# Optimization experiments

Measured on AMD Instinct MI355X. Metric: run time of the kernel, lower is better.

Reference implementation:

```python
import jax, jax.numpy as jnp
import numpy as np

N, T, F, H, DEG = 1024, 32, 128, 4, 32
HID, OUT = 512, 64
NNZ = N * DEG
D = F // H


def setup_inputs() -> dict:
    key = jax.random.key(0)
    ks = jax.random.split(key, 40)
    p = lambda i, shape, s=0.05: (jax.random.normal(ks[i], shape, dtype=jnp.float32) * s)
    inp = {
        'A_rows': jnp.repeat(jnp.arange(N, dtype=jnp.int32), DEG),
        'A_cols': jax.random.randint(ks[0], (NNZ,), 0, N, dtype=jnp.int32),
        'A_vals': jax.random.uniform(ks[1], (NNZ,), dtype=jnp.float32) / DEG,
        'X': jax.random.normal(ks[2], (N, T, F), dtype=jnp.float32),
        'W_gcn': p(3, (F, F)),
        'W_ih': p(4, (3 * F, F)), 'W_hh': p(5, (3 * F, F)),
        'b_ih': p(6, (3 * F,)), 'b_hh': p(7, (3 * F,)),
        'in_proj_w': p(8, (3 * F, F)), 'in_proj_b': p(9, (3 * F,)),
        'out_proj_w': p(10, (F, F)), 'out_proj_b': p(11, (F,)),
        'ln1_g': jnp.ones((F,), jnp.float32), 'ln1_b': jnp.zeros((F,), jnp.float32),
        'ln2_g': jnp.ones((F,), jnp.float32), 'ln2_b': jnp.zeros((F,), jnp.float32),
        'lnf_g': jnp.ones((F,), jnp.float32), 'lnf_b': jnp.zeros((F,), jnp.float32),
        'ff1_w': p(12, (HID, F)), 'ff1_b': p(13, (HID,)),
        'ff2_w': p(14, (F, HID)), 'ff2_b': p(15, (F,)),
        'fc1_w': p(16, (HID, T * F)), 'fc1_b': p(17, (HID,)),
        'fc2_w': p(18, (HID, HID)), 'fc2_b': p(19, (HID,)),
        'fc3_w': p(20, (OUT, HID)), 'fc3_b': p(21, (OUT,)),
    }
    return inp


def _pos_encoding():
    # pe[i, t] = sin(t / 10000**(2i/F)) for even t, cos(...) for odd t; constant over feature dim.
    i = jnp.arange(N, dtype=jnp.float32)
    t = jnp.arange(T, dtype=jnp.float32)
    inv = jnp.exp(-(2.0 * i / F) * jnp.log(jnp.float32(10000.0)))  # [N]
    ang = t[None, :] * inv[:, None]                                # [N, T]
    even = (jnp.arange(T) % 2 == 0)[None, :]
    return jnp.where(even, jnp.sin(ang), jnp.cos(ang))             # [N, T]


def _layer_norm(x, g, b, eps=1e-5):
    mu = x.mean(-1, keepdims=True)
    var = ((x - mu) ** 2).mean(-1, keepdims=True)
    return (x - mu) * jax.lax.rsqrt(var + eps) * g + b


def _forward(A_rows, A_cols, A_vals, X, W_gcn, W_ih, W_hh, b_ih, b_hh,
             in_proj_w, in_proj_b, out_proj_w, out_proj_b,
             ln1_g, ln1_b, ln2_g, ln2_b, lnf_g, lnf_b,
             ff1_w, ff1_b, ff2_w, ff2_b,
             fc1_w, fc1_b, fc2_w, fc2_b, fc3_w, fc3_b):
    def spmm(x2d):  # A_hat @ x2d via COO gather + segment-sum
        return jax.ops.segment_sum(A_vals[:, None] * x2d[A_cols], A_rows, num_segments=N)

    def gru_cell(x, h):  # torch GRUCell, gate order [r; z; n]
        gi = x @ W_ih.T + b_ih
        gh = h @ W_hh.T + b_hh
        ir, iz, inn = jnp.split(gi, 3, axis=-1)
        hr, hz, hn = jnp.split(gh, 3, axis=-1)
        r = jax.nn.sigmoid(ir + hr)
        z = jax.nn.sigmoid(iz + hz)
        n = jnp.tanh(inn + r * hn)
        return (1.0 - z) * n + z * h

    # GCN on full [N, T, F] block
    X_tilde = jax.nn.relu(spmm(X.reshape(N, T * F)).reshape(N, T, F) @ W_gcn)

    # sequential GRU + per-step GCN over time
    def step(h, x_t):
        g = gru_cell(x_t, h)                       # [N, F]
        h_new = jax.nn.relu(spmm(g) @ W_gcn)
        return h_new, g

    h0 = jnp.zeros((N, F), X.dtype)
    _, Hs = jax.lax.scan(step, h0, jnp.transpose(X_tilde, (1, 0, 2)))  # [T, N, F]
    Hm = jnp.transpose(Hs, (1, 0, 2)) + _pos_encoding()[:, :, None]    # [N, T, F]

    # TransformerEncoderLayer (post-norm, relu, dropout=0); seq axis = nodes, batch axis = T
    qkv = Hm @ in_proj_w.T + in_proj_b                 # [N, T, 3F]
    q, k, v = jnp.split(qkv, 3, axis=-1)
    q = q.reshape(N, T, H, D) * (1.0 / jnp.sqrt(jnp.float32(D)))
    k = k.reshape(N, T, H, D)
    v = v.reshape(N, T, H, D)
    scores = jnp.einsum('nthd,mthd->thnm', q, k)       # [T, H, N, N]
    attn = jax.nn.softmax(scores, axis=-1)
    ctx = jnp.einsum('thnm,mthd->nthd', attn, v).reshape(N, T, F)
    attn_out = ctx @ out_proj_w.T + out_proj_b
    x1 = _layer_norm(Hm + attn_out, ln1_g, ln1_b)
    ff = jax.nn.relu(x1 @ ff1_w.T + ff1_b) @ ff2_w.T + ff2_b
    x2 = _layer_norm(x1 + ff, ln2_g, ln2_b)
    enc = _layer_norm(x2, lnf_g, lnf_b)                # final encoder norm

    # MLP head
    flat = enc.reshape(N, T * F)
    h1 = jax.nn.relu(flat @ fc1_w.T + fc1_b)
    h2 = jax.nn.relu(h1 @ fc2_w.T + fc2_b)
    return h2 @ fc3_w.T + fc3_b                        # [N, OUT]


def reference(A_rows, A_cols, A_vals, X, W_gcn, W_ih, W_hh, b_ih, b_hh,
              in_proj_w, in_proj_b, out_proj_w, out_proj_b,
              ln1_g, ln1_b, ln2_g, ln2_b, lnf_g, lnf_b,
              ff1_w, ff1_b, ff2_w, ff2_b,
              fc1_w, fc1_b, fc2_w, fc2_b, fc3_w, fc3_b):
    return _forward(A_rows, A_cols, A_vals, X, W_gcn, W_ih, W_hh, b_ih, b_hh,
                    in_proj_w, in_proj_b, out_proj_w, out_proj_b,
                    ln1_g, ln1_b, ln2_g, ln2_b, lnf_g, lnf_b,
                    ff1_w, ff1_b, ff2_w, ff2_b,
                    fc1_w, fc1_b, fc2_w, fc2_b, fc3_w, fc3_b)
```

## Files before the change

### kernel.cpp

```cpp
#include <hip/hip_runtime.h>
#include <hip/hip_bf16.h>
#include <math.h>

#define N_NODES 1024
#define T_STEPS 32
#define F_DIM   128
#define H_HEADS 4
#define D_HEAD  32
#define DEG     32
#define HID     512
#define OUT_DIM 64
#define TF      (T_STEPS * F_DIM)
#define NT      (N_NODES * T_STEPS)
#define F3      (3 * F_DIM)

typedef __attribute__((ext_vector_type(8))) __bf16 bf16x8;
typedef __attribute__((ext_vector_type(4))) float  f32x4;

__device__ __forceinline__ short f2bf(float x) {
    union { float f; unsigned u; } v; v.f = x;
    unsigned r = (v.u + 0x7FFFu + ((v.u >> 16) & 1u)) >> 16;
    return (short)r;
}

__global__ void zero_kernel(float* p, int n) {
    int i = blockIdx.x * 256 + threadIdx.x;
    if (i < n) p[i] = 0.f;
}

template <bool RELU>
__global__ void bias_act(float* __restrict__ C, const float* __restrict__ bias,
                         int P, int total) {
    int i = blockIdx.x * 256 + threadIdx.x;
    if (i < total) {
        float v = C[i] + bias[i & (P - 1)];
        if (RELU) v = fmaxf(v, 0.f);
        C[i] = v;
    }
}

__global__ void transpose_whh(const float* __restrict__ W, float* __restrict__ WT) {
    int idx = blockIdx.x * 256 + threadIdx.x;
    if (idx < F3 * F_DIM) {
        int j = idx / F_DIM;
        int k = idx % F_DIM;
        WT[k * F3 + j] = W[idx];
    }
}

__global__ void spmm_wide(const int* __restrict__ cols, const float* __restrict__ vals,
                          const float* __restrict__ X, float* __restrict__ Y) {
    int n = blockIdx.y;
    int c = blockIdx.x * 256 + threadIdx.x;
    const int*   ce = cols + n * DEG;
    const float* ve = vals + n * DEG;
    float acc = 0.f;
#pragma unroll
    for (int e = 0; e < DEG; ++e) acc += ve[e] * X[ce[e] * TF + c];
    Y[n * TF + c] = acc;
}

__global__ __launch_bounds__(256) void gates_kernel(
        const float* __restrict__ GI, const float* __restrict__ GH,
        const float* __restrict__ h, const float* __restrict__ b_hh,
        float* __restrict__ g_out, float* __restrict__ Hm, int t) {
    int idx = blockIdx.x * 256 + threadIdx.x;
    int n = idx >> 7, f = idx & 127;
    size_t gib = ((size_t)n * T_STEPS + t) * F3;
    size_t ghb = (size_t)n * F3;
    float ir  = GI[gib + f];
    float iz  = GI[gib + 128 + f];
    float inn = GI[gib + 256 + f];
    float hr  = GH[ghb + f]       + b_hh[f];
    float hz  = GH[ghb + 128 + f] + b_hh[128 + f];
    float hn  = GH[ghb + 256 + f] + b_hh[256 + f];
    float hv  = h[idx];
    float rr = 1.f / (1.f + expf(-(ir + hr)));
    float zz = 1.f / (1.f + expf(-(iz + hz)));
    float nn = tanhf(inn + rr * hn);
    float g  = (1.f - zz) * nn + zz * hv;
    g_out[idx] = g;
    float inv = __expf(-(float)n * (9.210340371976184f / 64.0f));
    float ang = (float)t * inv;
    float pe  = ((t & 1) == 0) ? sinf(ang) : cosf(ang);
    Hm[((size_t)n * T_STEPS + t) * F_DIM + f] = g + pe;
}

__global__ __launch_bounds__(256) void scan_step(
        const int* __restrict__ cols, const float* __restrict__ vals,
        const float* __restrict__ g_in, const float* __restrict__ Wg,
        const float* __restrict__ WhhT, const float* __restrict__ b_hh,
        const float* __restrict__ GI, float* __restrict__ g_out,
        float* __restrict__ Hm, int t_next) {
    __shared__ float sp[2][F_DIM];
    __shared__ float hsn[2][F_DIM];
    __shared__ float part[2][F_DIM][8];
    __shared__ float gpart[2][2][F_DIM];
    int tid = threadIdx.x;
    int n0 = blockIdx.x * 2;
    int f = tid & 127, half = tid >> 7;
    float b0 = 0.f, b1 = 0.f;
    int eb = half * 16;
#pragma unroll
    for (int e = 0; e < 16; ++e) {
        int i0 = n0 * DEG + eb + e;
        int i1 = (n0 + 1) * DEG + eb + e;
        b0 += vals[i0] * g_in[cols[i0] * F_DIM + f];
        b1 += vals[i1] * g_in[cols[i1] * F_DIM + f];
    }
    gpart[half][0][f] = b0; gpart[half][1][f] = b1;
    __syncthreads();
    sp[half][f] = gpart[0][half][f] + gpart[1][half][f];
    __syncthreads();
    float c0 = 0.f, c1 = 0.f;
    int kb = half * 64;
#pragma unroll 4
    for (int k = 0; k < 64; ++k) {
        int kk = kb + k;
        float w = Wg[kk * F_DIM + f];
        c0 += sp[0][kk] * w; c1 += sp[1][kk] * w;
    }
    gpart[half][0][f] = c0; gpart[half][1][f] = c1;
    __syncthreads();
    {
        float hv = fmaxf(gpart[0][half][f] + gpart[1][half][f], 0.f);
        hsn[half][f] = hv;
    }
    __syncthreads();
    float a[6] = {0.f, 0.f, 0.f, 0.f, 0.f, 0.f};
#pragma unroll 2
    for (int k = 0; k < 64; ++k) {
        int kk = kb + k;
        const float* w = WhhT + kk * F3;
        float wr = w[f], wz = w[128 + f], wn = w[256 + f];
        float h0 = hsn[0][kk], h1 = hsn[1][kk];
        a[0] += h0 * wr; a[1] += h0 * wz; a[2] += h0 * wn;
        a[3] += h1 * wr; a[4] += h1 * wz; a[5] += h1 * wn;
    }
#pragma unroll
    for (int i = 0; i < 6; ++i) part[half][f][i] = a[i];
    __syncthreads();
    {
        int node = n0 + half;
        float ghr = part[0][f][half * 3 + 0] + part[1][f][half * 3 + 0] + b_hh[f];
        float ghz = part[0][f][half * 3 + 1] + part[1][f][half * 3 + 1] + b_hh[128 + f];
        float ghn = part[0][f][half * 3 + 2] + part[1][f][half * 3 + 2] + b_hh[256 + f];
        size_t gib = ((size_t)node * T_STEPS + t_next) * F3;
        float hv = hsn[half][f];
        float rr = 1.f / (1.f + expf(-(GI[gib + f] + ghr)));
        float zz = 1.f / (1.f + expf(-(GI[gib + 128 + f] + ghz)));
        float nn = tanhf(GI[gib + 256 + f] + rr * ghn);
        float g  = (1.f - zz) * nn + zz * hv;
        g_out[node * F_DIM + f] = g;
        float inv = __expf(-(float)node * (9.210340371976184f / 64.0f));
        float ang = (float)t_next * inv;
        float pe  = ((t_next & 1) == 0) ? sinf(ang) : cosf(ang);
        Hm[((size_t)node * T_STEPS + t_next) * F_DIM + f] = g + pe;
    }
}

__global__ __launch_bounds__(256) void qkv_gemm(const float* __restrict__ A,
                                                const float* __restrict__ B,
                                                const float* __restrict__ bias,
                                                short* __restrict__ Qb,
                                                short* __restrict__ Kb,
                                                short* __restrict__ VTb) {
    __shared__ short As[64][40];
    __shared__ short Bs[64][40];
    int tid = threadIdx.x;
    int p0 = blockIdx.x * 64, row0 = blockIdx.y * 64;
    int lane = tid & 63, w = tid >> 6, col = lane & 15, quad = lane >> 4;
    f32x4 acc[4];
#pragma unroll
    for (int j = 0; j < 4; ++j) acc[j] = (f32x4){0.f, 0.f, 0.f, 0.f};
    for (int k0 = 0; k0 < F_DIM; k0 += 32) {
#pragma unroll
        for (int i = 0; i < 2; ++i) {
            int idx = tid * 2 + i;
            int r = idx >> 3, c4 = (idx & 7) << 2;
            const float4 f4 = *(const float4*)(A + (size_t)(row0 + r) * F_DIM + k0 + c4);
            union { __hip_bfloat162 h2[2]; short4 s4; } u;
            u.h2[0] = __float22bfloat162_rn(make_float2(f4.x, f4.y));
            u.h2[1] = __float22bfloat162_rn(make_float2(f4.z, f4.w));
            *(short4*)&As[r][c4] = u.s4;
        }
#pragma unroll
        for (int i = 0; i < 2; ++i) {
            int idx = tid * 2 + i;
            int r = idx >> 3, c4 = (idx & 7) << 2;
            const float4 f4 = *(const float4*)(B + (size_t)(p0 + r) * F_DIM + k0 + c4);
            union { __hip_bfloat162 h2[2]; short4 s4; } u;
            u.h2[0] = __float22bfloat162_rn(make_float2(f4.x, f4.y));
            u.h2[1] = __float22bfloat162_rn(make_float2(f4.z, f4.w));
            *(short4*)&Bs[r][c4] = u.s4;
        }
        __syncthreads();
        bf16x8 af = *(const bf16x8*)&As[w * 16 + col][quad * 8];
#pragma unroll
        for (int j = 0; j < 4; ++j) {
            bf16x8 bv = *(const bf16x8*)&Bs[j * 16 + col][quad * 8];
            acc[j] = __builtin_amdgcn_mfma_f32_16x16x32_bf16(af, bv, acc[j], 0, 0, 0);
        }
        __syncthreads();
    }
#pragma unroll
    for (int j = 0; j < 4; ++j) {
        int cg = p0 + j * 16 + col;
        int which = cg >> 7, f = cg & 127;
        int hh = f >> 5, d = f & 31;
        float bv = bias[cg];
#pragma unroll
        for (int r = 0; r < 4; ++r) {
            int rg = row0 + w * 16 + quad * 4 + r;
            int n = rg >> 5, t = rg & 31;
            int th = t * H_HEADS + hh;
            float v = acc[j][r] + bv;
            if (which == 0)
                Qb[((size_t)th * N_NODES + n) * D_HEAD + d] = f2bf(v * 0.17677669529663687f);
            else if (which == 1)
                Kb[((size_t)th * N_NODES + n) * D_HEAD + d] = f2bf(v);
            else
                VTb[((size_t)th * D_HEAD + d) * N_NODES + n] = f2bf(v);
        }
    }
}

__global__ __launch_bounds__(64) void attn_mfma(const short* __restrict__ Qb,
                                                const short* __restrict__ Kb,
                                                const short* __restrict__ VTb,
                                                float* __restrict__ ctx) {
    int th = blockIdx.x;
    int t = th >> 2, hh = th & 3;
    int q0 = blockIdx.y * 16;
    int lane = threadIdx.x;
    int col  = lane & 15;
    int quad = lane >> 4;
    __shared__ short Ps[16][40];

    bf16x8 qf = *(const bf16x8*)(Qb + ((size_t)(th * N_NODES + q0 + col)) * D_HEAD + quad * 8);
    const short* Kbase = Kb  + (size_t)th * (N_NODES * D_HEAD);
    const short* Vbase = VTb + (size_t)th * (D_HEAD * N_NODES);

    f32x4 o0 = {0.f, 0.f, 0.f, 0.f}, o1 = {0.f, 0.f, 0.f, 0.f};
    float lr0 = 0.f, lr1 = 0.f, lr2 = 0.f, lr3 = 0.f;
    const f32x4 zc = {0.f, 0.f, 0.f, 0.f};

    for (int mt = 0; mt < 32; ++mt) {
        int m0 = mt * 32;
        bf16x8 k0 = *(const bf16x8*)(Kbase + (size_t)(m0 + col) * D_HEAD + quad * 8);
        bf16x8 k1 = *(const bf16x8*)(Kbase + (size_t)(m0 + 16 + col) * D_HEAD + quad * 8);
        f32x4 s0 = __builtin_amdgcn_mfma_f32_16x16x32_bf16(qf, k0, zc, 0, 0, 0);
        f32x4 s1 = __builtin_amdgcn_mfma_f32_16x16x32_bf16(qf, k1, zc, 0, 0, 0);
        float p0[4], p1[4];
#pragma unroll
        for (int r = 0; r < 4; ++r) {
            p0[r] = __expf(fminf(s0[r], 80.f));
            p1[r] = __expf(fminf(s1[r], 80.f));
        }
        lr0 += p0[0] + p1[0]; lr1 += p0[1] + p1[1];
        lr2 += p0[2] + p1[2]; lr3 += p0[3] + p1[3];
        __syncthreads();
#pragma unroll
        for (int r = 0; r < 4; ++r) {
            Ps[quad * 4 + r][col]      = f2bf(p0[r]);
            Ps[quad * 4 + r][col + 16] = f2bf(p1[r]);
        }
        __syncthreads();
        bf16x8 pf = *(const bf16x8*)(&Ps[col][quad * 8]);
        bf16x8 v0 = *(const bf16x8*)(Vbase + (size_t)col * N_NODES + m0 + quad * 8);
        bf16x8 v1 = *(const bf16x8*)(Vbase + (size_t)(col + 16) * N_NODES + m0 + quad * 8);
        o0 = __builtin_amdgcn_mfma_f32_16x16x32_bf16(pf, v0, o0, 0, 0, 0);
        o1 = __builtin_amdgcn_mfma_f32_16x16x32_bf16(pf, v1, o1, 0, 0, 0);
    }
    float lr[4] = {lr0, lr1, lr2, lr3};
#pragma unroll
    for (int r = 0; r < 4; ++r) {
        float s = lr[r];
        s += __shfl_xor(s, 1); s += __shfl_xor(s, 2);
        s += __shfl_xor(s, 4); s += __shfl_xor(s, 8);
        lr[r] = 1.f / s;
    }
#pragma unroll
    for (int r = 0; r < 4; ++r) {
        int n = q0 + quad * 4 + r;
        size_t base = ((size_t)n * T_STEPS + t) * F_DIM + hh * D_HEAD;
        ctx[base + col]      = o0[r] * lr[r];
        ctx[base + 16 + col] = o1[r] * lr[r];
    }
}

__global__ void ln_kernel(const float* __restrict__ a, const float* __restrict__ resid,
                          const float* __restrict__ gamma, const float* __restrict__ beta,
                          float* __restrict__ out) {
    int row = blockIdx.x;
    int tid = threadIdx.x;
    int base = row * F_DIM;
    float x0 = a[base + tid], x1 = a[base + 64 + tid];
    if (resid) { x0 += resid[base + tid]; x1 += resid[base + 64 + tid]; }
    float s = x0 + x1;
#pragma unroll
    for (int o = 32; o > 0; o >>= 1) s += __shfl_xor(s, o);
    float mu = s * (1.f / 128.f);
    float d0 = x0 - mu, d1 = x1 - mu;
    float v = d0 * d0 + d1 * d1;
#pragma unroll
    for (int o = 32; o > 0; o >>= 1) v += __shfl_xor(v, o);
    float inv = rsqrtf(v * (1.f / 128.f) + 1e-5f);
    out[base + tid]      = d0 * inv * gamma[tid] + beta[tid];
    out[base + 64 + tid] = d1 * inv * gamma[64 + tid] + beta[64 + tid];
}

template <bool TB, bool RELU, bool SPLITK>
__global__ __launch_bounds__(256) void mfma_gemm(const float* __restrict__ A,
                                                 const float* __restrict__ B,
                                                 const float* __restrict__ bias,
                                                 float* __restrict__ C,
                                                 int M, int K, int P, int Kc) {
    __shared__ short As[64][40];
    __shared__ short Bs[64][40];
    int tid = threadIdx.x;
    int p0 = blockIdx.x * 64, row0 = blockIdx.y * 64;
    int k_begin = SPLITK ? blockIdx.z * Kc : 0;
    int k_end   = SPLITK ? k_begin + Kc : K;
    int lane = tid & 63, w = tid >> 6, col = lane & 15, quad = lane >> 4;
    f32x4 acc[4];
#pragma unroll
    for (int j = 0; j < 4; ++j) acc[j] = (f32x4){0.f, 0.f, 0.f, 0.f};

    for (int k0 = k_begin; k0 < k_end; k0 += 32) {
#pragma unroll
        for (int i = 0; i < 2; ++i) {
            int idx = tid * 2 + i;
            int r = idx >> 3, c4 = (idx & 7) << 2;
            const float4 f4 = *(const float4*)(A + (size_t)(row0 + r) * K + k0 + c4);
            union { __hip_bfloat162 h2[2]; short4 s4; } u;
            u.h2[0] = __float22bfloat162_rn(make_float2(f4.x, f4.y));
            u.h2[1] = __float22bfloat162_rn(make_float2(f4.z, f4.w));
            *(short4*)&As[r][c4] = u.s4;
        }
        if (TB) {
#pragma unroll
            for (int i = 0; i < 2; ++i) {
                int idx = tid * 2 + i;
                int r = idx >> 3, c4 = (idx & 7) << 2;
                const float4 f4 = *(const float4*)(B + (size_t)(p0 + r) * K + k0 + c4);
                union { __hip_bfloat162 h2[2]; short4 s4; } u;
                u.h2[0] = __float22bfloat162_rn(make_float2(f4.x, f4.y));
                u.h2[1] = __float22bfloat162_rn(make_float2(f4.z, f4.w));
                *(short4*)&Bs[r][c4] = u.s4;
            }
        } else {
#pragma unroll
            for (int i = 0; i < 2; ++i) {
                int idx = tid * 2 + i;
                int kk = idx >> 4, c4 = (idx & 15) << 2;
                const float4 f4 = *(const float4*)(B + (size_t)(k0 + kk) * P + p0 + c4);
                Bs[c4 + 0][kk] = f2bf(f4.x);
                Bs[c4 + 1][kk] = f2bf(f4.y);
                Bs[c4 + 2][kk] = f2bf(f4.z);
                Bs[c4 + 3][kk] = f2bf(f4.w);
            }
        }
        __syncthreads();
        bf16x8 af = *(const bf16x8*)&As[w * 16 + col][quad * 8];
#pragma unroll
        for (int j = 0; j < 4; ++j) {
            bf16x8 bv = *(const bf16x8*)&Bs[j * 16 + col][quad * 8];
            acc[j] = __builtin_amdgcn_mfma_f32_16x16x32_bf16(af, bv, acc[j], 0, 0, 0);
        }
        __syncthreads();
    }
#pragma unroll
    for (int j = 0; j < 4; ++j) {
        int cg_ = p0 + j * 16 + col;
        float bvv = (!SPLITK && bias) ? bias[cg_] : 0.f;
#pragma unroll
        for (int r = 0; r < 4; ++r) {
            int rg = row0 + w * 16 + quad * 4 + r;
            if (SPLITK) {
                atomicAdd(&C[(size_t)rg * P + cg_], acc[j][r]);
            } else {
                float v = acc[j][r] + bvv;
                if (RELU) v = fmaxf(v, 0.f);
                C[(size_t)rg * P + cg_] = v;
            }
        }
    }
}

extern "C" void kernel_launch(void* const* d_in, const int* in_sizes, int n_in,
                              void* d_out, int out_size, void* d_ws, size_t ws_size,
                              hipStream_t stream) {
    const int*   A_cols     = (const int*)d_in[1];
    const float* A_vals     = (const float*)d_in[2];
    const float* X          = (const float*)d_in[3];
    const float* W_gcn      = (const float*)d_in[4];
    const float* W_ih       = (const float*)d_in[5];
    const float* W_hh       = (const float*)d_in[6];
    const float* b_ih       = (const float*)d_in[7];
    const float* b_hh       = (const float*)d_in[8];
    const float* in_proj_w  = (const float*)d_in[9];
    const float* in_proj_b  = (const float*)d_in[10];
    const float* out_proj_w = (const float*)d_in[11];
    const float* out_proj_b = (const float*)d_in[12];
    const float* ln1_g = (const float*)d_in[13];
    const float* ln1_b = (const float*)d_in[14];
    const float* ln2_g = (const float*)d_in[15];
    const float* ln2_b = (const float*)d_in[16];
    const float* lnf_g = (const float*)d_in[17];
    const float* lnf_b = (const float*)d_in[18];
    const float* ff1_w = (const float*)d_in[19];
    const float* ff1_b = (const float*)d_in[20];
    const float* ff2_w = (const float*)d_in[21];
    const float* ff2_b = (const float*)d_in[22];
    const float* fc1_w = (const float*)d_in[23];
    const float* fc1_b = (const float*)d_in[24];
    const float* fc2_w = (const float*)d_in[25];
    const float* fc2_b = (const float*)d_in[26];
    const float* fc3_w = (const float*)d_in[27];
    const float* fc3_b = (const float*)d_in[28];
    float* out = (float*)d_out;
    float* ws  = (float*)d_ws;

    const size_t o_Hm = 0;
    const size_t o_A  = o_Hm + 4194304;
    const size_t o_B  = o_A + 4194304;
    const size_t o_C  = o_B + 4194304;
    const size_t o_D  = o_C + 12582912;
    const size_t o_WT = o_D + 12582912;
    const size_t o_h  = o_WT + 49152;
    const size_t o_g  = o_h + 131072;
    const size_t o_h1 = o_g + 131072;
    const size_t o_h2 = o_h1 + 524288;

    float* Hm    = ws + o_Hm;
    float* bufA  = ws + o_A;
    float* bufB  = ws + o_B;
    float* bufC  = ws + o_C;
    float* GHz   = ws + o_D;
    short* Qb    = (short*)(ws + o_D);
    short* Kb    = Qb + 4194304;
    short* VTb   = Kb + 4194304;
    float* WhhT  = ws + o_WT;
    float* hbuf  = ws + o_h;
    float* g0    = ws + o_g;
    float* h1    = ws + o_h1;
    float* h2    = ws + o_h2;
    float* g1    = h2;

    spmm_wide<<<dim3(16, 1024), 256, 0, stream>>>(A_cols, A_vals, X, bufA);
    mfma_gemm<false, true, false><<<dim3(2, 512), 256, 0, stream>>>(bufA, W_gcn, nullptr, bufB, NT, F_DIM, F_DIM, 0);
    mfma_gemm<true, false, false><<<dim3(6, 512), 256, 0, stream>>>(bufB, W_ih, b_ih, bufC, NT, F_DIM, F3, 0);
    transpose_whh<<<192, 256, 0, stream>>>(W_hh, WhhT);
    zero_kernel<<<512, 256, 0, stream>>>(hbuf, 131072);
    zero_kernel<<<1536, 256, 0, stream>>>(GHz, 393216);
    gates_kernel<<<512, 256, 0, stream>>>(bufC, GHz, hbuf, b_hh, g0, Hm, 0);
    for (int s = 0; s < T_STEPS - 1; ++s) {
        const float* gi = (s & 1) ? g1 : g0;
        float*       go = (s & 1) ? g0 : g1;
        scan_step<<<512, 256, 0, stream>>>(A_cols, A_vals, gi, W_gcn, WhhT, b_hh, bufC, go, Hm, s + 1);
    }
    qkv_gemm<<<dim3(6, 512), 256, 0, stream>>>(Hm, in_proj_w, in_proj_b, Qb, Kb, VTb);
    attn_mfma<<<dim3(128, 64), 64, 0, stream>>>(Qb, Kb, VTb, bufA);
    mfma_gemm<true, false, false><<<dim3(2, 512), 256, 0, stream>>>(bufA, out_proj_w, out_proj_b, bufB, NT, F_DIM, F_DIM, 0);
    ln_kernel<<<NT, 64, 0, stream>>>(Hm, bufB, ln1_g, ln1_b, bufA);
    mfma_gemm<true, true, false><<<dim3(8, 512), 256, 0, stream>>>(bufA, ff1_w, ff1_b, bufC, NT, F_DIM, HID, 0);
    mfma_gemm<true, false, false><<<dim3(2, 512), 256, 0, stream>>>(bufC, ff2_w, ff2_b, bufB, NT, HID, F_DIM, 0);
    ln_kernel<<<NT, 64, 0, stream>>>(bufA, bufB, ln2_g, ln2_b, Hm);
    ln_kernel<<<NT, 64, 0, stream>>>(Hm, nullptr, lnf_g, lnf_b, bufA);
    zero_kernel<<<2048, 256, 0, stream>>>(h1, 524288);
    mfma_gemm<true, false, true><<<dim3(8, 16, 4), 256, 0, stream>>>(bufA, fc1_w, nullptr, h1, N_NODES, TF, HID, 1024);
    bias_act<true><<<2048, 256, 0, stream>>>(h1, fc1_b, HID, 524288);
    zero_kernel<<<2048, 256, 0, stream>>>(h2, 524288);
    mfma_gemm<true, false, true><<<dim3(8, 16, 4), 256, 0, stream>>>(h1, fc2_w, nullptr, h2, N_NODES, HID, HID, 128);
    bias_act<true><<<2048, 256, 0, stream>>>(h2, fc2_b, HID, 524288);
    zero_kernel<<<256, 256, 0, stream>>>(out, 65536);
    mfma_gemm<true, false, true><<<dim3(1, 16, 8), 256, 0, stream>>>(h2, fc3_w, nullptr, out, N_NODES, HID, OUT_DIM, 64);
    bias_act<false><<<256, 256, 0, stream>>>(out, fc3_b, OUT_DIM, 65536);
}
```

Baseline: 816.4 us.

## Batch four nodes per scan block with bf16 weights and trim small launches

The recurrent scan step now handles four nodes per block instead of two. Each weight load from W_gcn and W_hh is reused across four nodes, and both weights are pre-converted to bf16 by a merged prep kernel to halve their load traffic. The first GRU step gets its own kernel that assumes a zero hidden state, which removes two zero-fill launches and the GH buffer. Layer norm now packs four rows per 256-thread block, and the attention softmax uses a paired float-to-bf16 conversion. The trade-offs are reduced weight precision in the recurrence, fewer scan blocks (256), and higher register pressure from 12 accumulators.

New measurement: 869.9 us. 1.07x slower.

```diff
diff --git a/kernel.cpp b/kernel.cpp
--- a/kernel.cpp
+++ b/kernel.cpp
@@ -22,6 +22,9 @@
     unsigned r = (v.u + 0x7FFFu + ((v.u >> 16) & 1u)) >> 16;
     return (short)r;
 }
+__device__ __forceinline__ float bf2f(unsigned short b) {
+    union { unsigned u; float f; } v; v.u = ((unsigned)b) << 16; return v.f;
+}
 
 __global__ void zero_kernel(float* p, int n) {
     int i = blockIdx.x * 256 + threadIdx.x;
@@ -39,12 +42,17 @@
     }
 }
 
-__global__ void transpose_whh(const float* __restrict__ W, float* __restrict__ WT) {
+__global__ void prep_weights(const float* __restrict__ W_hh, const float* __restrict__ W_gcn,
+                             unsigned short* __restrict__ WhhT_bf,
+                             unsigned short* __restrict__ Wg_bf) {
     int idx = blockIdx.x * 256 + threadIdx.x;
     if (idx < F3 * F_DIM) {
         int j = idx / F_DIM;
         int k = idx % F_DIM;
-        WT[k * F3 + j] = W[idx];
+        WhhT_bf[k * F3 + j] = (unsigned short)f2bf(W_hh[idx]);
+    }
+    if (idx < F_DIM * F_DIM) {
+        Wg_bf[idx] = (unsigned short)f2bf(W_gcn[idx]);
     }
 }
 
@@ -60,93 +68,94 @@
     Y[n * TF + c] = acc;
 }
 
-__global__ __launch_bounds__(256) void gates_kernel(
-        const float* __restrict__ GI, const float* __restrict__ GH,
-        const float* __restrict__ h, const float* __restrict__ b_hh,
-        float* __restrict__ g_out, float* __restrict__ Hm, int t) {
+__global__ __launch_bounds__(256) void gates0_kernel(
+        const float* __restrict__ GI, const float* __restrict__ b_hh,
+        float* __restrict__ g_out, float* __restrict__ Hm) {
     int idx = blockIdx.x * 256 + threadIdx.x;
     int n = idx >> 7, f = idx & 127;
-    size_t gib = ((size_t)n * T_STEPS + t) * F3;
-    size_t ghb = (size_t)n * F3;
-    float ir  = GI[gib + f];
-    float iz  = GI[gib + 128 + f];
-    float inn = GI[gib + 256 + f];
-    float hr  = GH[ghb + f]       + b_hh[f];
-    float hz  = GH[ghb + 128 + f] + b_hh[128 + f];
-    float hn  = GH[ghb + 256 + f] + b_hh[256 + f];
-    float hv  = h[idx];
-    float rr = 1.f / (1.f + expf(-(ir + hr)));
-    float zz = 1.f / (1.f + expf(-(iz + hz)));
-    float nn = tanhf(inn + rr * hn);
-    float g  = (1.f - zz) * nn + zz * hv;
+    size_t gib = (size_t)n * T_STEPS * F3;
+    float rr = 1.f / (1.f + expf(-(GI[gib + f] + b_hh[f])));
+    float zz = 1.f / (1.f + expf(-(GI[gib + 128 + f] + b_hh[128 + f])));
+    float nn = tanhf(GI[gib + 256 + f] + rr * b_hh[256 + f]);
+    float g  = (1.f - zz) * nn;
     g_out[idx] = g;
-    float inv = __expf(-(float)n * (9.210340371976184f / 64.0f));
-    float ang = (float)t * inv;
-    float pe  = ((t & 1) == 0) ? sinf(ang) : cosf(ang);
-    Hm[((size_t)n * T_STEPS + t) * F_DIM + f] = g + pe;
+    Hm[(size_t)n * T_STEPS * F_DIM + f] = g;
 }
 
 __global__ __launch_bounds__(256) void scan_step(
         const int* __restrict__ cols, const float* __restrict__ vals,
-        const float* __restrict__ g_in, const float* __restrict__ Wg,
-        const float* __restrict__ WhhT, const float* __restrict__ b_hh,
+        const float* __restrict__ g_in, const unsigned short* __restrict__ Wg_bf,
+        const unsigned short* __restrict__ WhhT_bf, const float* __restrict__ b_hh,
         const float* __restrict__ GI, float* __restrict__ g_out,
         float* __restrict__ Hm, int t_next) {
-    __shared__ float sp[2][F_DIM];
-    __shared__ float hsn[2][F_DIM];
-    __shared__ float part[2][F_DIM][8];
-    __shared__ float gpart[2][2][F_DIM];
+    __shared__ float sp[4][F_DIM];
+    __shared__ float hsn[4][F_DIM];
+    __shared__ float part[2][F_DIM][13];
+    __shared__ float gpart[2][4][F_DIM];
     int tid = threadIdx.x;
-    int n0 = blockIdx.x * 2;
+    int n0 = blockIdx.x * 4;
     int f = tid & 127, half = tid >> 7;
-    float b0 = 0.f, b1 = 0.f;
+    float b4[4] = {0.f, 0.f, 0.f, 0.f};
     int eb = half * 16;
 #pragma unroll
-    for (int e = 0; e < 16; ++e) {
-        int i0 = n0 * DEG + eb + e;
-        int i1 = (n0 + 1) * DEG + eb + e;
-        b0 += vals[i0] * g_in[cols[i0] * F_DIM + f];
-        b1 += vals[i1] * g_in[cols[i1] * F_DIM + f];
-    }
-    gpart[half][0][f] = b0; gpart[half][1][f] = b1;
+    for (int j = 0; j < 4; ++j) {
+#pragma unroll
+        for (int e = 0; e < 16; ++e) {
+            int idx = (n0 + j) * DEG + eb + e;
+            b4[j] += vals[idx] * g_in[cols[idx] * F_DIM + f];
+        }
+    }
+#pragma unroll
+    for (int j = 0; j < 4; ++j) gpart[half][j][f] = b4[j];
     __syncthreads();
-    sp[half][f] = gpart[0][half][f] + gpart[1][half][f];
+    for (int idx = tid; idx < 512; idx += 256) {
+        int j = idx >> 7, ff = idx & 127;
+        sp[j][ff] = gpart[0][j][ff] + gpart[1][j][ff];
+    }
     __syncthreads();
-    float c0 = 0.f, c1 = 0.f;
     int kb = half * 64;
+    float c4[4] = {0.f, 0.f, 0.f, 0.f};
 #pragma unroll 4
     for (int k = 0; k < 64; ++k) {
         int kk = kb + k;
-        float w = Wg[kk * F_DIM + f];
-        c0 += sp[0][kk] * w; c1 += sp[1][kk] * w;
-    }
-    gpart[half][0][f] = c0; gpart[half][1][f] = c1;
+        float w = bf2f(Wg_bf[kk * F_DIM + f]);
+        c4[0] += sp[0][kk] * w; c4[1] += sp[1][kk] * w;
+        c4[2] += sp[2][kk] * w; c4[3] += sp[3][kk] * w;
+    }
+#pragma unroll
+    for (int j = 0; j < 4; ++j) gpart[half][j][f] = c4[j];
     __syncthreads();
-    {
-        float hv = fmaxf(gpart[0][half][f] + gpart[1][half][f], 0.f);
-        hsn[half][f] = hv;
+    for (int idx = tid; idx < 512; idx += 256) {
+        int j = idx >> 7, ff = idx & 127;
+        hsn[j][ff] = fmaxf(gpart[0][j][ff] + gpart[1][j][ff], 0.f);
     }
     __syncthreads();
-    float a[6] = {0.f, 0.f, 0.f, 0.f, 0.f, 0.f};
+    float a[12];
+#pragma unroll
+    for (int i = 0; i < 12; ++i) a[i] = 0.f;
 #pragma unroll 2
     for (int k = 0; k < 64; ++k) {
         int kk = kb + k;
-        const float* w = WhhT + kk * F3;
-        float wr = w[f], wz = w[128 + f], wn = w[256 + f];
-        float h0 = hsn[0][kk], h1 = hsn[1][kk];
-        a[0] += h0 * wr; a[1] += h0 * wz; a[2] += h0 * wn;
-        a[3] += h1 * wr; a[4] += h1 * wz; a[5] += h1 * wn;
-    }
-#pragma unroll
-    for (int i = 0; i < 6; ++i) part[half][f][i] = a[i];
+        const unsigned short* w = WhhT_bf + kk * F3;
+        float wr = bf2f(w[f]), wz = bf2f(w[128 + f]), wn = bf2f(w[256 + f]);
+        float h0 = hsn[0][kk], h1 = hsn[1][kk], h2 = hsn[2][kk], h3 = hsn[3][kk];
+        a[0] += h0 * wr; a[1]  += h0 * wz; a[2]  += h0 * wn;
+        a[3] += h1 * wr; a[4]  += h1 * wz; a[5]  += h1 * wn;
+        a[6] += h2 * wr; a[7]  += h2 * wz; a[8]  += h2 * wn;
+        a[9] += h3 * wr; a[10] += h3 * wz; a[11] += h3 * wn;
+    }
+#pragma unroll
+    for (int i = 0; i < 12; ++i) part[half][f][i] = a[i];
     __syncthreads();
-    {
-        int node = n0 + half;
-        float ghr = part[0][f][half * 3 + 0] + part[1][f][half * 3 + 0] + b_hh[f];
-        float ghz = part[0][f][half * 3 + 1] + part[1][f][half * 3 + 1] + b_hh[128 + f];
-        float ghn = part[0][f][half * 3 + 2] + part[1][f][half * 3 + 2] + b_hh[256 + f];
+#pragma unroll
+    for (int jj = 0; jj < 2; ++jj) {
+        int j = half * 2 + jj;
+        int node = n0 + j;
+        float ghr = part[0][f][j * 3 + 0] + part[1][f][j * 3 + 0] + b_hh[f];
+        float ghz = part[0][f][j * 3 + 1] + part[1][f][j * 3 + 1] + b_hh[128 + f];
+        float ghn = part[0][f][j * 3 + 2] + part[1][f][j * 3 + 2] + b_hh[256 + f];
         size_t gib = ((size_t)node * T_STEPS + t_next) * F3;
-        float hv = hsn[half][f];
+        float hv = hsn[j][f];
         float rr = 1.f / (1.f + expf(-(GI[gib + f] + ghr)));
         float zz = 1.f / (1.f + expf(-(GI[gib + 128 + f] + ghz)));
         float nn = tanhf(GI[gib + 256 + f] + rr * ghn);
@@ -262,8 +271,10 @@
         __syncthreads();
 #pragma unroll
         for (int r = 0; r < 4; ++r) {
-            Ps[quad * 4 + r][col]      = f2bf(p0[r]);
-            Ps[quad * 4 + r][col + 16] = f2bf(p1[r]);
+            union { __hip_bfloat162 h; short2 s; } u;
+            u.h = __float22bfloat162_rn(make_float2(p0[r], p1[r]));
+            Ps[quad * 4 + r][col]      = u.s.x;
+            Ps[quad * 4 + r][col + 16] = u.s.y;
         }
         __syncthreads();
         bf16x8 pf = *(const bf16x8*)(&Ps[col][quad * 8]);
@@ -289,11 +300,12 @@
     }
 }
 
-__global__ void ln_kernel(const float* __restrict__ a, const float* __restrict__ resid,
-                          const float* __restrict__ gamma, const float* __restrict__ beta,
-                          float* __restrict__ out) {
-    int row = blockIdx.x;
-    int tid = threadIdx.x;
+__global__ __launch_bounds__(256) void ln_kernel(
+        const float* __restrict__ a, const float* __restrict__ resid,
+        const float* __restrict__ gamma, const float* __restrict__ beta,
+        float* __restrict__ out) {
+    int row = blockIdx.x * 4 + (threadIdx.x >> 6);
+    int tid = threadIdx.x & 63;
     int base = row * F_DIM;
     float x0 = a[base + tid], x1 = a[base + 64 + tid];
     if (resid) { x0 += resid[base + tid]; x1 += resid[base + 64 + tid]; }
@@ -437,12 +449,11 @@
     float* bufA  = ws + o_A;
     float* bufB  = ws + o_B;
     float* bufC  = ws + o_C;
-    float* GHz   = ws + o_D;
     short* Qb    = (short*)(ws + o_D);
     short* Kb    = Qb + 4194304;
     short* VTb   = Kb + 4194304;
-    float* WhhT  = ws + o_WT;
-    float* hbuf  = ws + o_h;
+    unsigned short* WhhT_bf = (unsigned short*)(ws + o_WT);
+    unsigned short* Wg_bf   = WhhT_bf + 49152;
     float* g0    = ws + o_g;
     float* h1    = ws + o_h1;
     float* h2    = ws + o_h2;
@@ -451,23 +462,21 @@
     spmm_wide<<<dim3(16, 1024), 256, 0, stream>>>(A_cols, A_vals, X, bufA);
     mfma_gemm<false, true, false><<<dim3(2, 512), 256, 0, stream>>>(bufA, W_gcn, nullptr, bufB, NT, F_DIM, F_DIM, 0);
     mfma_gemm<true, false, false><<<dim3(6, 512), 256, 0, stream>>>(bufB, W_ih, b_ih, bufC, NT, F_DIM, F3, 0);
-    transpose_whh<<<192, 256, 0, stream>>>(W_hh, WhhT);
-    zero_kernel<<<512, 256, 0, stream>>>(hbuf, 131072);
-    zero_kernel<<<1536, 256, 0, stream>>>(GHz, 393216);
-    gates_kernel<<<512, 256, 0, stream>>>(bufC, GHz, hbuf, b_hh, g0, Hm, 0);
+    prep_weights<<<192, 256, 0, stream>>>(W_hh, W_gcn, WhhT_bf, Wg_bf);
+    gates0_kernel<<<512, 256, 0, stream>>>(bufC, b_hh, g0, Hm);
     for (int s = 0; s < T_STEPS - 1; ++s) {
         const float* gi = (s & 1) ? g1 : g0;
         float*       go = (s & 1) ? g0 : g1;
-        scan_step<<<512, 256, 0, stream>>>(A_cols, A_vals, gi, W_gcn, WhhT, b_hh, bufC, go, Hm, s + 1);
+        scan_step<<<256, 256, 0, stream>>>(A_cols, A_vals, gi, Wg_bf, WhhT_bf, b_hh, bufC, go, Hm, s + 1);
     }
     qkv_gemm<<<dim3(6, 512), 256, 0, stream>>>(Hm, in_proj_w, in_proj_b, Qb, Kb, VTb);
     attn_mfma<<<dim3(128, 64), 64, 0, stream>>>(Qb, Kb, VTb, bufA);
     mfma_gemm<true, false, false><<<dim3(2, 512), 256, 0, stream>>>(bufA, out_proj_w, out_proj_b, bufB, NT, F_DIM, F_DIM, 0);
-    ln_kernel<<<NT, 64, 0, stream>>>(Hm, bufB, ln1_g, ln1_b, bufA);
+    ln_kernel<<<NT / 4, 256, 0, stream>>>(Hm, bufB, ln1_g, ln1_b, bufA);
     mfma_gemm<true, true, false><<<dim3(8, 512), 256, 0, stream>>>(bufA, ff1_w, ff1_b, bufC, NT, F_DIM, HID, 0);
     mfma_gemm<true, false, false><<<dim3(2, 512), 256, 0, stream>>>(bufC, ff2_w, ff2_b, bufB, NT, HID, F_DIM, 0);
-    ln_kernel<<<NT, 64, 0, stream>>>(bufA, bufB, ln2_g, ln2_b, Hm);
-    ln_kernel<<<NT, 64, 0, stream>>>(Hm, nullptr, lnf_g, lnf_b, bufA);
+    ln_kernel<<<NT / 4, 256, 0, stream>>>(bufA, bufB, ln2_g, ln2_b, Hm);
+    ln_kernel<<<NT / 4, 256, 0, stream>>>(Hm, nullptr, lnf_g, lnf_b, bufA);
     zero_kernel<<<2048, 256, 0, stream>>>(h1, 524288);
     mfma_gemm<true, false, true><<<dim3(8, 16, 4), 256, 0, stream>>>(bufA, fc1_w, nullptr, h1, N_NODES, TF, HID, 1024);
     bias_act<true><<<2048, 256, 0, stream>>>(h1, fc1_b, HID, 524288);
```
